# Kernel tuning notes

Hardware: AMD Instinct MI355X
Metric: run time of the kernel (lower is better)

Reference implementation:

```python
import jax, jax.numpy as jnp
import numpy as np

BATCH, IN_F, OUT_F = 8192, 4096, 4096


def setup_inputs() -> dict:
    key = jax.random.key(0)
    kx, kw = jax.random.split(key)
    x = jax.random.normal(kx, (BATCH, IN_F), dtype=jnp.float32)
    # weights binarized to {-1, +1} as in __init__ (uniform(-1,1) then sign)
    W = jnp.where(jax.random.normal(kw, (OUT_F, IN_F)) > 0, 1.0, -1.0).astype(jnp.float32)
    return {"x": x, "W": W}


def reference(x, W):
    # forward: input thresholded to {0,1} (x>0 -> 1, else 0), then x_bin @ W^T, no bias
    x_bin = (x > 0).astype(x.dtype)
    return jnp.matmul(x_bin, W.T)  # [batch, out_features]
```

## Files before the change

kernel.cpp:

```cpp
#include <hip/hip_runtime.h>
#include <stdint.h>

typedef __attribute__((ext_vector_type(4))) int   v4i;
typedef __attribute__((ext_vector_type(8))) int   v8i;
typedef __attribute__((ext_vector_type(4))) float v4f;

#define BATCH 8192
#define KDIM  4096
#define NOUT  4096
#define KB    (KDIM / 2)

__global__ __launch_bounds__(256) void pack_x4(const float* __restrict__ x,
                                               uint32_t* __restrict__ xb) {
    int t = blockIdx.x * 256 + threadIdx.x;
    const float4* p = (const float4*)x + (size_t)t * 2;
    float4 f0 = p[0];
    float4 f1 = p[1];
    uint32_t b = (f0.x > 0.f ? 0x2u        : 0u)
               | (f0.y > 0.f ? 0x20u       : 0u)
               | (f0.z > 0.f ? 0x200u      : 0u)
               | (f0.w > 0.f ? 0x2000u     : 0u)
               | (f1.x > 0.f ? 0x20000u    : 0u)
               | (f1.y > 0.f ? 0x200000u   : 0u)
               | (f1.z > 0.f ? 0x2000000u  : 0u)
               | (f1.w > 0.f ? 0x20000000u : 0u);
    xb[t] = b;
}

__global__ __launch_bounds__(256) void pack_w4(const float* __restrict__ w,
                                               uint32_t* __restrict__ wb) {
    int t = blockIdx.x * 256 + threadIdx.x;
    const float4* p = (const float4*)w + (size_t)t * 2;
    float4 f0 = p[0];
    float4 f1 = p[1];
    uint32_t b = (f0.x > 0.f ? 0x2u        : 0xAu)
               | (f0.y > 0.f ? 0x20u       : 0xA0u)
               | (f0.z > 0.f ? 0x200u      : 0xA00u)
               | (f0.w > 0.f ? 0x2000u     : 0xA000u)
               | (f1.x > 0.f ? 0x20000u    : 0xA0000u)
               | (f1.y > 0.f ? 0x200000u   : 0xA00000u)
               | (f1.z > 0.f ? 0x2000000u  : 0xA000000u)
               | (f1.w > 0.f ? 0x20000000u : 0xA0000000u);
    wb[t] = b;
}

__global__ __launch_bounds__(256) void bin_gemm4(const uint8_t* __restrict__ A,
                                                 const uint8_t* __restrict__ B,
                                                 float* __restrict__ C) {
    __shared__ __align__(16) uint8_t smA[128 * 64];
    __shared__ __align__(16) uint8_t smB[128 * 64];

    const int tid  = threadIdx.x;
    const int w    = tid >> 6;
    const int lane = tid & 63;
    const int q    = lane >> 4;
    const int mp   = lane & 15;

    const int Mbase = blockIdx.y * 128;
    const int Nbase = blockIdx.x * 128;
    const int wm = (w >> 1) * 64;
    const int wn = (w & 1) * 64;

    const int srow = lane >> 2;
    const int swz  = ((lane & 3) ^ ((lane >> 3) & 3)) * 16;
    const int g0   = (w * 2 + 0) * 16;
    const int g1   = (w * 2 + 1) * 16;

    const uint8_t* gA0 = A + (size_t)(Mbase + g0 + srow) * KB + swz;
    const uint8_t* gA1 = A + (size_t)(Mbase + g1 + srow) * KB + swz;
    const uint8_t* gB0 = B + (size_t)(Nbase + g0 + srow) * KB + swz;
    const uint8_t* gB1 = B + (size_t)(Nbase + g1 + srow) * KB + swz;

    auto lA0 = (__attribute__((address_space(3))) void*)(smA + g0 * 64);
    auto lA1 = (__attribute__((address_space(3))) void*)(smA + g1 * 64);
    auto lB0 = (__attribute__((address_space(3))) void*)(smB + g0 * 64);
    auto lB1 = (__attribute__((address_space(3))) void*)(smB + g1 * 64);

    const int slot = (q ^ ((mp >> 1) & 3)) * 16;

    v4f acc[4][4] = {};

    for (int kt = 0; kt < KDIM / 128; ++kt) {
        const int kof = kt * 64;
        __builtin_amdgcn_global_load_lds(
            (__attribute__((address_space(1))) void*)(gA0 + kof), lA0, 16, 0, 0);
        __builtin_amdgcn_global_load_lds(
            (__attribute__((address_space(1))) void*)(gA1 + kof), lA1, 16, 0, 0);
        __builtin_amdgcn_global_load_lds(
            (__attribute__((address_space(1))) void*)(gB0 + kof), lB0, 16, 0, 0);
        __builtin_amdgcn_global_load_lds(
            (__attribute__((address_space(1))) void*)(gB1 + kof), lB1, 16, 0, 0);
        __syncthreads();

        v4i af[4], bf[4];
        #pragma unroll
        for (int i = 0; i < 4; ++i)
            af[i] = *(const v4i*)(smA + (wm + i * 16 + mp) * 64 + slot);
        #pragma unroll
        for (int i = 0; i < 4; ++i)
            bf[i] = *(const v4i*)(smB + (wn + i * 16 + mp) * 64 + slot);

        #pragma unroll
        for (int mi = 0; mi < 4; ++mi) {
            v8i a8 = {af[mi][0], af[mi][1], af[mi][2], af[mi][3], 0, 0, 0, 0};
            #pragma unroll
            for (int ni = 0; ni < 4; ++ni) {
                v8i b8 = {bf[ni][0], bf[ni][1], bf[ni][2], bf[ni][3], 0, 0, 0, 0};
                acc[mi][ni] = __builtin_amdgcn_mfma_scale_f32_16x16x128_f8f6f4(
                    a8, b8, acc[mi][ni], 4, 4,
                    0, 0x7F7F7F7F, 0, 0x7F7F7F7F);
            }
        }
        __syncthreads();
    }

    float* Cp = C + (size_t)(Mbase + wm + q * 4) * NOUT + (Nbase + wn + mp);
    #pragma unroll
    for (int mi = 0; mi < 4; ++mi)
        #pragma unroll
        for (int ni = 0; ni < 4; ++ni)
            #pragma unroll
            for (int r = 0; r < 4; ++r)
                Cp[(size_t)(mi * 16 + r) * NOUT + ni * 16] = acc[mi][ni][r];
}

extern "C" void kernel_launch(void* const* d_in, const int* in_sizes, int n_in,
                              void* d_out, int out_size, void* d_ws, size_t ws_size,
                              hipStream_t stream) {
    const float* x = (const float*)d_in[0];
    const float* W = (const float*)d_in[1];
    float* out = (float*)d_out;

    uint8_t* xb = (uint8_t*)d_ws;
    uint8_t* wb = (uint8_t*)d_ws + (size_t)BATCH * KDIM / 2;

    pack_x4<<<(BATCH * (size_t)KDIM / 8) / 256, 256, 0, stream>>>(x, (uint32_t*)xb);
    pack_w4<<<((size_t)NOUT * KDIM / 8) / 256, 256, 0, stream>>>(W, (uint32_t*)wb);

    dim3 grid(NOUT / 128, BATCH / 128);
    bin_gemm4<<<grid, 256, 0, stream>>>(xb, wb, out);
}
```

Before: 333.1 us.

## Enlarge binary GEMM tile to 256x256 with double-buffered LDS prefetch

Each block of the FP4 MFMA GEMM now computes a 256x256 output tile with 8 waves instead of 128x128 with 4 waves. It loads a 256-element K slice per stage into a 128KB double-buffered LDS area, with an 8-way XOR swizzle. The next stage's global-to-LDS loads are issued before the current stage's MFMAs, which hides load latency and halves the number of barriers. The bigger tile also doubles operand reuse per byte loaded. In exchange, the large LDS footprint limits the GPU to one block per CU, the 32 accumulator tiles per wave add register pressure, and the grid shrinks to 512 blocks.

```diff
diff --git a/kernel.cpp b/kernel.cpp
--- a/kernel.cpp
+++ b/kernel.cpp
@@ -9,6 +9,8 @@
 #define KDIM  4096
 #define NOUT  4096
 #define KB    (KDIM / 2)
+#define BK_B  128
+#define NT    (KDIM / 256)
 
 __global__ __launch_bounds__(256) void pack_x4(const float* __restrict__ x,
                                                uint32_t* __restrict__ xb) {
@@ -44,11 +46,10 @@
     wb[t] = b;
 }
 
-__global__ __launch_bounds__(256) void bin_gemm4(const uint8_t* __restrict__ A,
-                                                 const uint8_t* __restrict__ B,
-                                                 float* __restrict__ C) {
-    __shared__ __align__(16) uint8_t smA[128 * 64];
-    __shared__ __align__(16) uint8_t smB[128 * 64];
+__global__ __launch_bounds__(512, 2) void bin_gemm4(const uint8_t* __restrict__ A,
+                                                    const uint8_t* __restrict__ B,
+                                                    float* __restrict__ C) {
+    __shared__ __align__(16) uint8_t sm[131072];
 
     const int tid  = threadIdx.x;
     const int w    = tid >> 6;
@@ -56,67 +57,92 @@
     const int q    = lane >> 4;
     const int mp   = lane & 15;
 
-    const int Mbase = blockIdx.y * 128;
-    const int Nbase = blockIdx.x * 128;
-    const int wm = (w >> 1) * 64;
-    const int wn = (w & 1) * 64;
+    const int Mbase = blockIdx.y * 256;
+    const int Nbase = blockIdx.x * 256;
+    const int wm = (w >> 2) * 128;
+    const int wn = (w & 3) * 64;
 
-    const int srow = lane >> 2;
-    const int swz  = ((lane & 3) ^ ((lane >> 3) & 3)) * 16;
-    const int g0   = (w * 2 + 0) * 16;
-    const int g1   = (w * 2 + 1) * 16;
+    const int srow = w * 8 + (lane >> 3);
+    const int swz  = ((lane & 7) ^ ((lane >> 3) & 7)) * 16;
 
-    const uint8_t* gA0 = A + (size_t)(Mbase + g0 + srow) * KB + swz;
-    const uint8_t* gA1 = A + (size_t)(Mbase + g1 + srow) * KB + swz;
-    const uint8_t* gB0 = B + (size_t)(Nbase + g0 + srow) * KB + swz;
-    const uint8_t* gB1 = B + (size_t)(Nbase + g1 + srow) * KB + swz;
+    const uint8_t* pA = A + (size_t)(Mbase + srow) * KB + swz;
+    const uint8_t* pB = B + (size_t)(Nbase + srow) * KB + swz;
+    const int ldsw = w * 1024;
 
-    auto lA0 = (__attribute__((address_space(3))) void*)(smA + g0 * 64);
-    auto lA1 = (__attribute__((address_space(3))) void*)(smA + g1 * 64);
-    auto lB0 = (__attribute__((address_space(3))) void*)(smB + g0 * 64);
-    auto lB1 = (__attribute__((address_space(3))) void*)(smB + g1 * 64);
+    const int rsw = mp & 7;
 
-    const int slot = (q ^ ((mp >> 1) & 3)) * 16;
+    v4f acc[8][4] = {};
 
-    v4f acc[4][4] = {};
+    #pragma unroll
+    for (int L = 0; L < 4; ++L) {
+        __builtin_amdgcn_global_load_lds(
+            (__attribute__((address_space(1))) void*)(pA + (size_t)(L * 64) * KB),
+            (__attribute__((address_space(3))) void*)(sm + L * 8192 + ldsw), 16, 0, 0);
+        __builtin_amdgcn_global_load_lds(
+            (__attribute__((address_space(1))) void*)(pB + (size_t)(L * 64) * KB),
+            (__attribute__((address_space(3))) void*)(sm + 32768 + L * 8192 + ldsw), 16, 0, 0);
+    }
+    __syncthreads();
 
-    for (int kt = 0; kt < KDIM / 128; ++kt) {
-        const int kof = kt * 64;
-        __builtin_amdgcn_global_load_lds(
-            (__attribute__((address_space(1))) void*)(gA0 + kof), lA0, 16, 0, 0);
-        __builtin_amdgcn_global_load_lds(
-            (__attribute__((address_space(1))) void*)(gA1 + kof), lA1, 16, 0, 0);
-        __builtin_amdgcn_global_load_lds(
-            (__attribute__((address_space(1))) void*)(gB0 + kof), lB0, 16, 0, 0);
-        __builtin_amdgcn_global_load_lds(
-            (__attribute__((address_space(1))) void*)(gB1 + kof), lB1, 16, 0, 0);
-        __syncthreads();
+    for (int t = 0; t < NT; ++t) {
+        if (t + 1 < NT) {
+            const int nb  = (t + 1) & 1;
+            const int kof = (t + 1) * BK_B;
+            #pragma unroll
+            for (int L = 0; L < 4; ++L) {
+                __builtin_amdgcn_global_load_lds(
+                    (__attribute__((address_space(1))) void*)(pA + (size_t)(L * 64) * KB + kof),
+                    (__attribute__((address_space(3))) void*)(sm + nb * 65536 + L * 8192 + ldsw),
+                    16, 0, 0);
+                __builtin_amdgcn_global_load_lds(
+                    (__attribute__((address_space(1))) void*)(pB + (size_t)(L * 64) * KB + kof),
+                    (__attribute__((address_space(3))) void*)(sm + nb * 65536 + 32768 + L * 8192 + ldsw),
+                    16, 0, 0);
+            }
+        }
 
-        v4i af[4], bf[4];
+        const uint8_t* sA = sm + (t & 1) * 65536;
+        const uint8_t* sB = sA + 32768;
+
+        v4i bfr[4][2];
         #pragma unroll
-        for (int i = 0; i < 4; ++i)
-            af[i] = *(const v4i*)(smA + (wm + i * 16 + mp) * 64 + slot);
-        #pragma unroll
-        for (int i = 0; i < 4; ++i)
-            bf[i] = *(const v4i*)(smB + (wn + i * 16 + mp) * 64 + slot);
+        for (int ni = 0; ni < 4; ++ni)
+            #pragma unroll
+            for (int ks = 0; ks < 2; ++ks)
+                bfr[ni][ks] = *(const v4i*)(sB + (wn + ni * 16 + mp) * 128
+                                            + ((ks * 4 + q) ^ rsw) * 16);
 
         #pragma unroll
-        for (int mi = 0; mi < 4; ++mi) {
-            v8i a8 = {af[mi][0], af[mi][1], af[mi][2], af[mi][3], 0, 0, 0, 0};
+        for (int p = 0; p < 4; ++p) {
+            v4i afr[2][2];
             #pragma unroll
-            for (int ni = 0; ni < 4; ++ni) {
-                v8i b8 = {bf[ni][0], bf[ni][1], bf[ni][2], bf[ni][3], 0, 0, 0, 0};
-                acc[mi][ni] = __builtin_amdgcn_mfma_scale_f32_16x16x128_f8f6f4(
-                    a8, b8, acc[mi][ni], 4, 4,
-                    0, 0x7F7F7F7F, 0, 0x7F7F7F7F);
-            }
+            for (int i = 0; i < 2; ++i)
+                #pragma unroll
+                for (int ks = 0; ks < 2; ++ks)
+                    afr[i][ks] = *(const v4i*)(sA + (wm + (p * 2 + i) * 16 + mp) * 128
+                                               + ((ks * 4 + q) ^ rsw) * 16);
+            #pragma unroll
+            for (int i = 0; i < 2; ++i)
+                #pragma unroll
+                for (int ni = 0; ni < 4; ++ni)
+                    #pragma unroll
+                    for (int ks = 0; ks < 2; ++ks) {
+                        v8i a8 = {afr[i][ks][0], afr[i][ks][1], afr[i][ks][2], afr[i][ks][3],
+                                  0, 0, 0, 0};
+                        v8i b8 = {bfr[ni][ks][0], bfr[ni][ks][1], bfr[ni][ks][2],
+                                  bfr[ni][ks][3], 0, 0, 0, 0};
+                        acc[p * 2 + i][ni] = __builtin_amdgcn_mfma_scale_f32_16x16x128_f8f6f4(
+                            a8, b8, acc[p * 2 + i][ni], 4, 4,
+                            0, 0x7F7F7F7F, 0, 0x7F7F7F7F);
+                    }
         }
+
         __syncthreads();
     }
 
     float* Cp = C + (size_t)(Mbase + wm + q * 4) * NOUT + (Nbase + wn + mp);
     #pragma unroll
-    for (int mi = 0; mi < 4; ++mi)
+    for (int mi = 0; mi < 8; ++mi)
         #pragma unroll
         for (int ni = 0; ni < 4; ++ni)
             #pragma unroll
@@ -137,6 +163,6 @@
     pack_x4<<<(BATCH * (size_t)KDIM / 8) / 256, 256, 0, stream>>>(x, (uint32_t*)xb);
     pack_w4<<<((size_t)NOUT * KDIM / 8) / 256, 256, 0, stream>>>(W, (uint32_t*)wb);
 
-    dim3 grid(NOUT / 128, BATCH / 128);
-    bin_gemm4<<<grid, 256, 0, stream>>>(xb, wb, out);
+    dim3 grid(NOUT / 256, BATCH / 256);
+    bin_gemm4<<<grid, 512, 0, stream>>>(xb, wb, out);
 }
```

New measurement: 322.7 us. -3.1%, faster.
